# Kernel tuning notes

Hardware: AMD Instinct MI355X
Metric: run time of the kernel (lower is better)

Reference implementation:

```python
import jax, jax.numpy as jnp
import numpy as np

N, E, H, C, IN = 20000, 640000, 4, 64, 256
HC = H * C
NEG_SLOPE = 0.2


def setup_inputs() -> dict:
    key = jax.random.key(0)
    ks = jax.random.split(key, 24)
    rn = lambda k, s: jax.random.normal(k, s, jnp.float32) * 0.05
    return {
        "x": jax.random.normal(ks[0], (N, IN), jnp.float32),
        "edge_index": jax.random.randint(ks[1], (2, E), 0, N),
        "confidence": jax.random.normal(ks[2], (N,), jnp.float32),
        "w_in": rn(ks[3], (IN, C)), "b_in": jnp.zeros((C,), jnp.float32),
        "lin_w0": rn(ks[4], (C, HC)),
        "lin_w12": rn(ks[5], (2, HC, HC)),
        "att_src": rn(ks[6], (3, H, C)),
        "att_dst": rn(ks[7], (3, H, C)),
        "gat_bias": jnp.zeros((3, HC), jnp.float32),
        "conf_w": rn(ks[8], (HC, 1)), "conf_b": jnp.zeros((1,), jnp.float32),
        "nc_w1": rn(ks[9], (HC, C)), "nc_b1": jnp.zeros((C,), jnp.float32),
        "nc_w2": rn(ks[10], (C, 1)), "nc_b2": jnp.zeros((1,), jnp.float32),
        "oc_w1": rn(ks[11], (HC, C)), "oc_b1": jnp.zeros((C,), jnp.float32),
        "oc_w2": rn(ks[12], (C, 1)), "oc_b2": jnp.zeros((1,), jnp.float32),
        "ec_w1": rn(ks[13], (HC, C)), "ec_b1": jnp.zeros((C,), jnp.float32),
        "ec_w2": rn(ks[14], (C, 4)), "ec_b2": jnp.zeros((4,), jnp.float32),
    }


def _gat_layer(h_in, src, dst, n, lin_w, a_src, a_dst, bias):
    # h_in: (n, in_ch). PyG GATConv: linear -> per-edge attn -> segment softmax -> scatter-add.
    h = (h_in @ lin_w).reshape(n, H, C)
    s_src = jnp.einsum("nhc,hc->nh", h, a_src)  # (n, H)
    s_dst = jnp.einsum("nhc,hc->nh", h, a_dst)
    alpha = jax.nn.leaky_relu(s_src[src] + s_dst[dst], NEG_SLOPE)  # (E', H)
    # softmax over incoming edges of each dst node (self-loops guarantee coverage)
    amax = jax.ops.segment_max(alpha, dst, num_segments=n)
    ex = jnp.exp(alpha - amax[dst])
    denom = jax.ops.segment_sum(ex, dst, num_segments=n)
    coef = ex / jnp.maximum(denom[dst], 1e-16)
    msg = h[src] * coef[:, :, None]  # (E', H, C)
    out = jax.ops.segment_sum(msg, dst, num_segments=n)
    return out.reshape(n, HC) + bias


def reference(x, edge_index, confidence, w_in, b_in, lin_w0, lin_w12,
              att_src, att_dst, gat_bias, conf_w, conf_b,
              nc_w1, nc_b1, nc_w2, nc_b2, oc_w1, oc_b1, oc_w2, oc_b2,
              ec_w1, ec_b1, ec_w2, ec_b2):
    n = x.shape[0]
    loops = jnp.arange(n)
    src = jnp.concatenate([edge_index[0], loops])  # PyG add_self_loops=True
    dst = jnp.concatenate([edge_index[1], loops])
    h = jax.nn.relu(x @ w_in + b_in)  # input_proj + relu (dropout off in eval)
    lin_ws = [lin_w0, lin_w12[0], lin_w12[1]]
    conf_norm = jax.nn.sigmoid(confidence)  # (n,)
    for i in range(3):
        h_new = _gat_layer(h, src, dst, n, lin_ws[i], att_src[i], att_dst[i], gat_bias[i])
        cw = jax.nn.sigmoid(h_new @ conf_w + conf_b)[:, 0] * conf_norm
        h_new = h_new * cw[:, None]
        h = h + h_new if h.shape[-1] == h_new.shape[-1] else h_new
        if i < 2:
            h = jax.nn.relu(h)
    mlp = lambda w1, b1, w2, b2: jax.nn.relu(h @ w1 + b1) @ w2 + b2
    node_pred = jax.nn.sigmoid(mlp(nc_w1, nc_b1, nc_w2, nc_b2))[:, 0]
    origin_pred = jax.nn.sigmoid(mlp(oc_w1, oc_b1, oc_w2, oc_b2))[:, 0]
    error_type_pred = mlp(ec_w1, ec_b1, ec_w2, ec_b2)
    return node_pred, origin_pred, error_type_pred, h
```

## Files before the change

### kernel.cpp

```cpp
#include <hip/hip_runtime.h>
#include <cstdint>
#include <cstddef>

#define NN   20000
#define NPAD 20224
#define EE   640000
#define E2   660000
#define HHD  4
#define CC   64
#define HC   256
#define NEG  0.2f

#define NBUK 313
#define NBLK 129
#define EPB  5120
#define SCN  (NBUK * NBLK)

typedef short bf16x8 __attribute__((ext_vector_type(8)));
typedef float f32x4 __attribute__((ext_vector_type(4)));

__device__ __forceinline__ float sigmoidf_(float x) { return 1.0f / (1.0f + __expf(-x)); }

__device__ __forceinline__ float wred_sum(float v) {
#pragma unroll
    for (int d = 32; d; d >>= 1) v += __shfl_xor(v, d, 64);
    return v;
}

__device__ __forceinline__ unsigned short f2bf(float f) {
    unsigned u = __float_as_uint(f);
    u = (u + 0x7fff + ((u >> 16) & 1)) >> 16;
    return (unsigned short)u;
}
__device__ __forceinline__ float bfval(unsigned short h) { return __uint_as_float(((unsigned)h) << 16); }
__device__ __forceinline__ float bf_lo(unsigned u) { return __uint_as_float(u << 16); }
__device__ __forceinline__ float bf_hi(unsigned u) { return __uint_as_float(u & 0xffff0000u); }

__global__ __launch_bounds__(256) void hist_edges(const int* __restrict__ ei,
                                                  int* __restrict__ bhist) {
    __shared__ int h[NBUK];
    int bl = blockIdx.x, t = threadIdx.x;
    for (int i = t; i < NBUK; i += 256) h[i] = 0;
    __syncthreads();
    int e0 = bl * EPB;
#pragma unroll 4
    for (int i = t; i < EPB; i += 256) {
        int e = e0 + i;
        if (e < E2) {
            int d = (e < EE) ? ei[EE + e] : (e - EE);
            atomicAdd(&h[d >> 6], 1);
        }
    }
    __syncthreads();
    for (int i = t; i < NBUK; i += 256) bhist[i * NBLK + bl] = h[i];
}

__global__ __launch_bounds__(1024) void scan_hist(const int* __restrict__ bhist,
                                                  int* __restrict__ sbase) {
    __shared__ int buf[1024];
    int t = threadIdx.x;
    int base = t * 40;
    int local[40];
    int s = 0;
#pragma unroll
    for (int i = 0; i < 40; i++) {
        int idx = base + i;
        int v = (idx < SCN) ? bhist[idx] : 0;
        local[i] = v;
        s += v;
    }
    buf[t] = s;
    __syncthreads();
    for (int d = 1; d < 1024; d <<= 1) {
        int tv = (t >= d) ? buf[t - d] : 0;
        __syncthreads();
        buf[t] += tv;
        __syncthreads();
    }
    int run = buf[t] - s;
#pragma unroll
    for (int i = 0; i < 40; i++) {
        int idx = base + i;
        if (idx < SCN) sbase[idx] = run;
        run += local[i];
    }
}

__global__ __launch_bounds__(256) void scatter_bucket(const int* __restrict__ ei,
                                                      const int* __restrict__ sbase,
                                                      unsigned int* __restrict__ ebuf) {
    __shared__ int cur[NBUK];
    int bl = blockIdx.x, t = threadIdx.x;
    for (int i = t; i < NBUK; i += 256) cur[i] = sbase[i * NBLK + bl];
    __syncthreads();
    int e0 = bl * EPB;
#pragma unroll 4
    for (int i = t; i < EPB; i += 256) {
        int e = e0 + i;
        if (e < E2) {
            int s, d;
            if (e < EE) { s = ei[e]; d = ei[EE + e]; }
            else        { s = e - EE; d = s; }
            int p = atomicAdd(&cur[d >> 6], 1);
            ebuf[p] = ((unsigned int)(d & 63) << 15) | (unsigned int)s;
        }
    }
}

__global__ __launch_bounds__(256) void build_csr(const unsigned int* __restrict__ ebuf,
                                                 const int* __restrict__ sbase,
                                                 int* __restrict__ off,
                                                 int* __restrict__ csr) {
    __shared__ int hist[64], sc[64], curl[64];
    int bu = blockIdx.x, t = threadIdx.x;
    int base = sbase[bu * NBLK];
    int end  = (bu + 1 < NBUK) ? sbase[(bu + 1) * NBLK] : E2;
    int ne = end - base;
    if (t < 64) hist[t] = 0;
    __syncthreads();
    for (int i = t; i < ne; i += 256) {
        int dl = (int)(ebuf[base + i] >> 15);
        atomicAdd(&hist[dl], 1);
    }
    __syncthreads();
    if (t < 64) sc[t] = hist[t];
    __syncthreads();
    for (int d = 1; d < 64; d <<= 1) {
        int v = (t < 64 && t >= d) ? sc[t - d] : 0;
        __syncthreads();
        if (t < 64) sc[t] += v;
        __syncthreads();
    }
    int n0 = bu * 64;
    if (t < 64) {
        int ex = base + sc[t] - hist[t];
        if (n0 + t < NN) off[n0 + t] = ex;
        curl[t] = ex;
    }
    if (bu == NBUK - 1 && t == 0) off[NN] = E2;
    __syncthreads();
    for (int i = t; i < ne; i += 256) {
        unsigned int v = ebuf[base + i];
        int dl = (int)(v >> 15);
        int p = atomicAdd(&curl[dl], 1);
        csr[p] = (int)(v & 0x7fffu);
    }
}

#define WTOT 212992
__global__ void prep_inputs(const float* __restrict__ x,
                            const float* __restrict__ w_in, const float* __restrict__ lin_w0,
                            const float* __restrict__ lin_w12,
                            const float* __restrict__ nc1, const float* __restrict__ oc1,
                            const float* __restrict__ ec1,
                            const float* __restrict__ nb, const float* __restrict__ ob,
                            const float* __restrict__ eb,
                            unsigned short* __restrict__ whi,
                            float* __restrict__ bcat,
                            unsigned short* __restrict__ xh, unsigned short* __restrict__ xl) {
    int idx = blockIdx.x * 256 + threadIdx.x;
    if (idx < NN * 64) {
        float4 v = ((const float4*)x)[idx];
        ushort4 hi, lo;
        hi.x = f2bf(v.x); lo.x = f2bf(v.x - bfval(hi.x));
        hi.y = f2bf(v.y); lo.y = f2bf(v.y - bfval(hi.y));
        hi.z = f2bf(v.z); lo.z = f2bf(v.z - bfval(hi.z));
        hi.w = f2bf(v.w); lo.w = f2bf(v.w - bfval(hi.w));
        ((ushort4*)xh)[idx] = hi;
        ((ushort4*)xl)[idx] = lo;
    }
    if (idx < 192) {
        int g = idx >> 6, jj = idx & 63;
        const float* b = (g == 0) ? nb : ((g == 1) ? ob : eb);
        bcat[idx] = b[jj];
    }
    if (idx >= WTOT) return;
    float v;
    if (idx < 16384) {
        int n = idx >> 8, k = idx & 255;
        v = w_in[k * 64 + n];
    } else if (idx < 32768) {
        int r = idx - 16384;
        int n = r >> 6, k = r & 63;
        v = lin_w0[k * 256 + n];
    } else if (idx < 98304) {
        int r = idx - 32768;
        int n = r >> 8, k = r & 255;
        v = lin_w12[k * 256 + n];
    } else if (idx < 163840) {
        int r = idx - 98304;
        int n = r >> 8, k = r & 255;
        v = lin_w12[65536 + k * 256 + n];
    } else {
        int r = idx - 163840;
        int n = r >> 8, k = r & 255;
        int g = n >> 6, jj = n & 63;
        const float* w = (g == 0) ? nc1 : ((g == 1) ? oc1 : ec1);
        v = w[k * 64 + jj];
    }
    whi[idx] = f2bf(v);
}

template <int K, int OUT_CH, int MODE, int NT>
__global__ __launch_bounds__(256) void gemm_lds(
    const unsigned short* __restrict__ Ahp, const unsigned short* __restrict__ Alp,
    const unsigned short* __restrict__ Wh,
    const float* __restrict__ bias,
    unsigned short* __restrict__ Outh, unsigned short* __restrict__ Outl,
    const float* __restrict__ a_src, const float* __restrict__ a_dst,
    float* __restrict__ s_src, float* __restrict__ s_dst,
    const float* __restrict__ w2n, const float* __restrict__ w2o,
    const float* __restrict__ w2e,
    const float* __restrict__ b2n, const float* __restrict__ b2o,
    const float* __restrict__ b2e,
    float* __restrict__ outbuf, int nreal) {
    constexpr int LB = K + 8;
    constexpr int NS = K / 32;
    __shared__ unsigned short Bh[64 * LB];
    const int tid = threadIdx.x;
    const int wv = tid >> 6, lane = tid & 63;
    const int quad = lane >> 4, ln = lane & 15;
    const int mb = blockIdx.x * 64;
    const int r0 = mb + wv * 16 + ln;

    const unsigned short* aph = Ahp + (size_t)r0 * K + quad * 8;
    const unsigned short* apl = Alp + (size_t)r0 * K + quad * 8;
    bf16x8 ah[NS], al[NS];
#pragma unroll
    for (int s = 0; s < NS; s++) {
        ah[s] = *(const bf16x8*)(aph + s * 32);
        al[s] = *(const bf16x8*)(apl + s * 32);
    }

    for (int ct = 0; ct < NT; ct++) {
        const int cb = ct * 64;
        if (ct > 0) __syncthreads();

        constexpr int NCHK = 64 * (K / 8);
#pragma unroll
        for (int i = 0; i < NCHK / 256; i++) {
            int flat = tid + i * 256;
            int r = flat / (K / 8);
            int c = (flat % (K / 8)) * 8;
            *(uint4*)&Bh[r * LB + c] = *(const uint4*)&Wh[(size_t)(cb + r) * K + c];
        }
        __syncthreads();

        f32x4 acc[4];
#pragma unroll
        for (int j = 0; j < 4; j++) {
            acc[j][0] = 0.f; acc[j][1] = 0.f; acc[j][2] = 0.f; acc[j][3] = 0.f;
        }

#pragma unroll
        for (int s = 0; s < NS; s++) {
#pragma unroll
            for (int cg = 0; cg < 4; cg++) {
                bf16x8 bh = *(const bf16x8*)&Bh[(cg * 16 + ln) * LB + quad * 8 + s * 32];
                acc[cg] = __builtin_amdgcn_mfma_f32_16x16x32_bf16(ah[s], bh, acc[cg], 0, 0, 0);
                acc[cg] = __builtin_amdgcn_mfma_f32_16x16x32_bf16(al[s], bh, acc[cg], 0, 0, 0);
            }
        }

        if (MODE == 1) {
            float av[4], dv[4];
#pragma unroll
            for (int cg = 0; cg < 4; cg++) {
                av[cg] = a_src[cb + cg * 16 + ln];
                dv[cg] = a_dst[cb + cg * 16 + ln];
            }
#pragma unroll
            for (int reg = 0; reg < 4; reg++) {
                float ps = 0.f, pd = 0.f;
#pragma unroll
                for (int cg = 0; cg < 4; cg++) {
                    float t = acc[cg][reg];
                    ps += t * av[cg];
                    pd += t * dv[cg];
                }
#pragma unroll
                for (int d = 1; d < 16; d <<= 1) {
                    ps += __shfl_xor(ps, d, 64);
                    pd += __shfl_xor(pd, d, 64);
                }
                if (ln == 0) {
                    int row = mb + wv * 16 + quad * 4 + reg;
                    if (row < nreal) {
                        s_src[row * 4 + ct] = ps;
                        s_dst[row * 4 + ct] = pd;
                    }
                }
            }
        }

        if (MODE == 3) {
            float bv[4];
#pragma unroll
            for (int cg = 0; cg < 4; cg++) bv[cg] = bias[cb + cg * 16 + ln];
            if (ct < 2) {
                const float* w2 = (ct == 0) ? w2n : w2o;
                float b2 = (ct == 0) ? b2n[0] : b2o[0];
                float wv2[4];
#pragma unroll
                for (int cg = 0; cg < 4; cg++) wv2[cg] = w2[cg * 16 + ln];
#pragma unroll
                for (int reg = 0; reg < 4; reg++) {
                    float t = 0.f;
#pragma unroll
                    for (int cg = 0; cg < 4; cg++) {
                        float tv = fmaxf(acc[cg][reg] + bv[cg], 0.f);
                        t += tv * wv2[cg];
                    }
#pragma unroll
                    for (int d = 1; d < 16; d <<= 1) t += __shfl_xor(t, d, 64);
                    int row = mb + wv * 16 + quad * 4 + reg;
                    if (ln == 0 && row < nreal)
                        outbuf[ct * NN + row] = sigmoidf_(t + b2);
                }
            } else {
                float4 w4[4];
#pragma unroll
                for (int cg = 0; cg < 4; cg++) w4[cg] = ((const float4*)w2e)[cg * 16 + ln];
#pragma unroll
                for (int reg = 0; reg < 4; reg++) {
                    float e0 = 0.f, e1 = 0.f, e2 = 0.f, e3 = 0.f;
#pragma unroll
                    for (int cg = 0; cg < 4; cg++) {
                        float tv = fmaxf(acc[cg][reg] + bv[cg], 0.f);
                        e0 += tv * w4[cg].x; e1 += tv * w4[cg].y;
                        e2 += tv * w4[cg].z; e3 += tv * w4[cg].w;
                    }
#pragma unroll
                    for (int d = 1; d < 16; d <<= 1) {
                        e0 += __shfl_xor(e0, d, 64); e1 += __shfl_xor(e1, d, 64);
                        e2 += __shfl_xor(e2, d, 64); e3 += __shfl_xor(e3, d, 64);
                    }
                    int row = mb + wv * 16 + quad * 4 + reg;
                    if (ln == 0 && row < nreal) {
                        float4 ev = make_float4(e0 + b2e[0], e1 + b2e[1], e2 + b2e[2], e3 + b2e[3]);
                        *(float4*)&outbuf[2 * NN + row * 4] = ev;
                    }
                }
            }
            continue;
        }

#pragma unroll
        for (int cg = 0; cg < 4; cg++) {
            int col = cb + cg * 16 + ln;
            int rbase = mb + wv * 16 + quad * 4;
#pragma unroll
            for (int reg = 0; reg < 4; reg++) {
                float v = acc[cg][reg];
                int r = rbase + reg;
                if (MODE == 0) {
                    v += bias[col]; v = fmaxf(v, 0.f);
                    unsigned short hi = f2bf(v);
                    Outh[(size_t)r * OUT_CH + col] = hi;
                    Outl[(size_t)r * OUT_CH + col] = f2bf(v - bfval(hi));
                } else if (MODE == 1) {
                    Outh[(size_t)r * OUT_CH + col] = f2bf(v);
                }
            }
        }
    }
}

__global__ __launch_bounds__(256) void gat_node(const unsigned short* __restrict__ hhb,
                                                const float* __restrict__ s_src,
                                                const float* __restrict__ s_dst,
                                                const int* __restrict__ csr_src,
                                                const int* __restrict__ csr_off,
                                                const float* __restrict__ gbias,
                                                const float* __restrict__ conf_w,
                                                const float* __restrict__ conf_b,
                                                const float* __restrict__ confid,
                                                unsigned short* __restrict__ h_hi,
                                                unsigned short* __restrict__ h_lo,
                                                float* __restrict__ outbuf,
                                                int layer) {
    __shared__ float Lc[4][64];
    __shared__ int   Ls[4][16];
    int wv = threadIdx.x >> 6;
    int lane = threadIdx.x & 63;
    int n = blockIdx.x * 4 + wv;
    int myhead = lane >> 4, slot = lane & 15;
    int off0 = csr_off[n];
    int deg = csr_off[n + 1] - off0;
    const int* cp = csr_src + off0;
    const unsigned short* hrow = hhb + lane * 4;
    float sdm = s_dst[n * 4 + myhead];

    float ax = 0.f, ay = 0.f, az = 0.f, aw = 0.f, smp = 0.f;
    int nch = (deg + 15) >> 4;
    bool valid = slot < deg;
    int sl = cp[valid ? slot : deg - 1];
    float ssv = s_src[sl * 4 + myhead];
    for (int t = 0; t < nch; t++) {
        float a = ssv + sdm;
        a = a > 0.f ? a : NEG * a;
        float c = valid ? __expf(a) : 0.f;
        smp += c;
        Lc[wv][lane] = c;
        if (myhead == 0) Ls[wv][slot] = sl;
        __builtin_amdgcn_wave_barrier();
        float4 c0 = *(const float4*)&Lc[wv][myhead * 16 + 0];
        float4 c1 = *(const float4*)&Lc[wv][myhead * 16 + 4];
        float4 c2 = *(const float4*)&Lc[wv][myhead * 16 + 8];
        float4 c3 = *(const float4*)&Lc[wv][myhead * 16 + 12];
        int4 s0 = *(const int4*)&Ls[wv][0];
        int4 s1 = *(const int4*)&Ls[wv][4];
        int4 s2 = *(const int4*)&Ls[wv][8];
        int4 s3 = *(const int4*)&Ls[wv][12];
        __builtin_amdgcn_wave_barrier();
        if (t + 1 < nch) {
            int i = ((t + 1) << 4) + slot;
            valid = i < deg;
            sl = cp[valid ? i : deg - 1];
            ssv = s_src[sl * 4 + myhead];
        }
        float cf[16] = {c0.x, c0.y, c0.z, c0.w, c1.x, c1.y, c1.z, c1.w,
                        c2.x, c2.y, c2.z, c2.w, c3.x, c3.y, c3.z, c3.w};
        int sv[16] = {s0.x, s0.y, s0.z, s0.w, s1.x, s1.y, s1.z, s1.w,
                      s2.x, s2.y, s2.z, s2.w, s3.x, s3.y, s3.z, s3.w};
#pragma unroll
        for (int q = 0; q < 16; q++) {
            uint2 u = *(const uint2*)(hrow + ((size_t)sv[q] << 8));
            ax += cf[q] * bf_lo(u.x); ay += cf[q] * bf_hi(u.x);
            az += cf[q] * bf_lo(u.y); aw += cf[q] * bf_hi(u.y);
        }
    }
    smp += __shfl_xor(smp, 1, 64);
    smp += __shfl_xor(smp, 2, 64);
    smp += __shfl_xor(smp, 4, 64);
    smp += __shfl_xor(smp, 8, 64);
    float inv = 1.0f / fmaxf(smp, 1e-16f);
    ax *= inv; ay *= inv; az *= inv; aw *= inv;

    float4 b4 = *(const float4*)&gbias[lane * 4];
    float hx = ax + b4.x, hy = ay + b4.y, hz = az + b4.z, hw = aw + b4.w;
    float4 cw4 = *(const float4*)&conf_w[lane * 4];
    float local = hx * cw4.x + hy * cw4.y + hz * cw4.z + hw * cw4.w;
    float tot = wred_sum(local);
    float cw = sigmoidf_(tot + conf_b[0]) * sigmoidf_(confid[n]);
    hx *= cw; hy *= cw; hz *= cw; hw *= cw;
    if (layer > 0) {
        ushort4 ph = *(const ushort4*)&h_hi[(size_t)n * HC + lane * 4];
        ushort4 pl = *(const ushort4*)&h_lo[(size_t)n * HC + lane * 4];
        hx += bfval(ph.x) + bfval(pl.x);
        hy += bfval(ph.y) + bfval(pl.y);
        hz += bfval(ph.z) + bfval(pl.z);
        hw += bfval(ph.w) + bfval(pl.w);
    }
    if (layer < 2) {
        hx = fmaxf(hx, 0.f); hy = fmaxf(hy, 0.f);
        hz = fmaxf(hz, 0.f); hw = fmaxf(hw, 0.f);
    } else {
        *(float4*)&outbuf[6 * NN + (size_t)n * HC + lane * 4] =
            make_float4(hx, hy, hz, hw);
    }
    ushort4 oh, ol;
    oh.x = f2bf(hx); ol.x = f2bf(hx - bfval(oh.x));
    oh.y = f2bf(hy); ol.y = f2bf(hy - bfval(oh.y));
    oh.z = f2bf(hz); ol.z = f2bf(hz - bfval(oh.z));
    oh.w = f2bf(hw); ol.w = f2bf(hw - bfval(oh.w));
    *(ushort4*)&h_hi[(size_t)n * HC + lane * 4] = oh;
    *(ushort4*)&h_lo[(size_t)n * HC + lane * 4] = ol;
}

extern "C" void kernel_launch(void* const* d_in, const int* in_sizes, int n_in,
                              void* d_out, int out_size, void* d_ws, size_t ws_size,
                              hipStream_t stream) {
    const float* x       = (const float*)d_in[0];
    const int*   ei      = (const int*)d_in[1];
    const float* conf    = (const float*)d_in[2];
    const float* w_in    = (const float*)d_in[3];
    const float* b_in    = (const float*)d_in[4];
    const float* lin_w0  = (const float*)d_in[5];
    const float* lin_w12 = (const float*)d_in[6];
    const float* att_src = (const float*)d_in[7];
    const float* att_dst = (const float*)d_in[8];
    const float* gbias   = (const float*)d_in[9];
    const float* conf_w  = (const float*)d_in[10];
    const float* conf_b  = (const float*)d_in[11];
    const float* nc_w1   = (const float*)d_in[12];
    const float* nc_b1   = (const float*)d_in[13];
    const float* nc_w2   = (const float*)d_in[14];
    const float* nc_b2   = (const float*)d_in[15];
    const float* oc_w1   = (const float*)d_in[16];
    const float* oc_b1   = (const float*)d_in[17];
    const float* oc_w2   = (const float*)d_in[18];
    const float* oc_b2   = (const float*)d_in[19];
    const float* ec_w1   = (const float*)d_in[20];
    const float* ec_b1   = (const float*)d_in[21];
    const float* ec_w2   = (const float*)d_in[22];
    const float* ec_b2   = (const float*)d_in[23];
    float* out = (float*)d_out;

    char* p = (char*)d_ws;
    auto alloc = [&](size_t bytes) -> void* {
        void* r = (void*)p;
        p += (bytes + 255) & ~(size_t)255;
        return r;
    };
    unsigned short* h_hi = (unsigned short*)alloc((size_t)NPAD * HC * 2);
    unsigned short* h_lo = (unsigned short*)alloc((size_t)NPAD * HC * 2);
    unsigned short* hh   = (unsigned short*)alloc((size_t)NPAD * HC * 2);
    unsigned short* h0h  = (unsigned short*)alloc((size_t)NPAD * CC * 2);
    unsigned short* h0l  = (unsigned short*)alloc((size_t)NPAD * CC * 2);
    float*          ssrc = (float*)alloc((size_t)NN * 4 * 4);
    float*          sdst = (float*)alloc((size_t)NN * 4 * 4);
    int*            off  = (int*)alloc((size_t)(NN + 1) * 4);
    int*            csr  = (int*)alloc((size_t)E2 * 4);
    int*            bhist= (int*)alloc((size_t)SCN * 4);
    int*            sbase= (int*)alloc((size_t)SCN * 4);
    unsigned short* whi  = (unsigned short*)alloc((size_t)WTOT * 2);
    float*          bcat = (float*)alloc((size_t)192 * 4);
    unsigned short* xh   = (unsigned short*)alloc((size_t)NPAD * 256 * 2 * 2);
    unsigned short* xl   = xh + (size_t)NPAD * 256;
    unsigned int*   ebuf = (unsigned int*)xh;

    const unsigned short* wt_in = whi;
    const unsigned short* wt_l0 = whi + 16384;
    const unsigned short* wt_a  = whi + 32768;
    const unsigned short* wt_b  = whi + 98304;
    const unsigned short* wt_hd = whi + 163840;

    hist_edges<<<NBLK, 256, 0, stream>>>(ei, bhist);
    scan_hist<<<1, 1024, 0, stream>>>(bhist, sbase);
    scatter_bucket<<<NBLK, 256, 0, stream>>>(ei, sbase, ebuf);
    build_csr<<<NBUK, 256, 0, stream>>>(ebuf, sbase, off, csr);

    prep_inputs<<<(NN * 64 + 255) / 256, 256, 0, stream>>>(
        x, w_in, lin_w0, lin_w12, nc_w1, oc_w1, ec_w1, nc_b1, oc_b1, ec_b1,
        whi, bcat, xh, xl);

    gemm_lds<256, 64, 0, 1><<<dim3(NPAD / 64, 1), 256, 0, stream>>>(
        xh, xl, wt_in, b_in, h0h, h0l, nullptr, nullptr, nullptr, nullptr,
        nullptr, nullptr, nullptr, nullptr, nullptr, nullptr, nullptr, NN);

    gemm_lds<64, 256, 1, 4><<<dim3(NPAD / 64, 1), 256, 0, stream>>>(
        h0h, h0l, wt_l0, nullptr, hh, nullptr, att_src, att_dst, ssrc, sdst,
        nullptr, nullptr, nullptr, nullptr, nullptr, nullptr, nullptr, NN);
    gat_node<<<NN / 4, 256, 0, stream>>>(hh, ssrc, sdst, csr, off, gbias, conf_w, conf_b, conf,
                                         h_hi, h_lo, out, 0);

    for (int i = 1; i < 3; i++) {
        const unsigned short* wh = (i == 1) ? wt_a : wt_b;
        gemm_lds<256, 256, 1, 4><<<dim3(NPAD / 64, 1), 256, 0, stream>>>(
            h_hi, h_lo, wh, nullptr, hh, nullptr,
            att_src + i * HHD * CC, att_dst + i * HHD * CC, ssrc, sdst,
            nullptr, nullptr, nullptr, nullptr, nullptr, nullptr, nullptr, NN);
        gat_node<<<NN / 4, 256, 0, stream>>>(hh, ssrc, sdst, csr, off, gbias + i * HC,
                                             conf_w, conf_b, conf, h_hi, h_lo, out, i);
    }

    gemm_lds<256, 192, 3, 3><<<dim3(NPAD / 64, 1), 256, 0, stream>>>(
        h_hi, h_lo, wt_hd, bcat, nullptr, nullptr, nullptr, nullptr, nullptr, nullptr,
        nc_w2, oc_w2, ec_w2, nc_b2, oc_b2, ec_b2, out, NN);
}
```

Baseline: 386.0 us.

## Fuse all stages into one persistent kernel with grid-wide barriers

Replaces the sequence of about twelve kernel launches (CSR build, input prep, GEMMs, GAT aggregation, heads) with a single persistent kernel of 960 blocks. The kernel loops over virtual block indices and separates stages with atomic-counter grid barriers. Independent stages now share phases: prep runs with the histogram, the first GEMM with the scan, and the layer-0 GEMM with the scatter. This removes launch gaps and tail effects. The cost is a shared LDS footprint sized for the largest stage, which may lower occupancy, plus spin-wait barriers that deadlock if the 960 blocks cannot all be resident. The scan is reworked to 256 threads, and ebuf gets its own buffer instead of aliasing xh.

```diff
diff --git a/kernel.cpp b/kernel.cpp
--- a/kernel.cpp
+++ b/kernel.cpp
@@ -15,6 +15,9 @@
 #define NBLK 129
 #define EPB  5120
 #define SCN  (NBUK * NBLK)
+#define PREP_BLKS 5000
+#define GEMM_BLKS (NPAD / 64)
+#define GRID 960
 
 typedef short bf16x8 __attribute__((ext_vector_type(8)));
 typedef float f32x4 __attribute__((ext_vector_type(4)));
@@ -36,10 +39,21 @@
 __device__ __forceinline__ float bf_lo(unsigned u) { return __uint_as_float(u << 16); }
 __device__ __forceinline__ float bf_hi(unsigned u) { return __uint_as_float(u & 0xffff0000u); }
 
-__global__ __launch_bounds__(256) void hist_edges(const int* __restrict__ ei,
-                                                  int* __restrict__ bhist) {
-    __shared__ int h[NBUK];
-    int bl = blockIdx.x, t = threadIdx.x;
+__device__ __forceinline__ void gsync(int* bar, int target) {
+    __syncthreads();
+    if (threadIdx.x == 0) {
+        __threadfence();
+        atomicAdd(bar, 1);
+        while (atomicAdd(bar, 0) < target) __builtin_amdgcn_s_sleep(8);
+        __threadfence();
+    }
+    __syncthreads();
+}
+
+
+__device__ __forceinline__ void hist_body(int bl, const int* __restrict__ ei,
+                                          int* __restrict__ bhist, int* h ) {
+    int t = threadIdx.x;
     for (int i = t; i < NBUK; i += 256) h[i] = 0;
     __syncthreads();
     int e0 = bl * EPB;
@@ -53,44 +67,14 @@
     }
     __syncthreads();
     for (int i = t; i < NBUK; i += 256) bhist[i * NBLK + bl] = h[i];
-}
-
-__global__ __launch_bounds__(1024) void scan_hist(const int* __restrict__ bhist,
-                                                  int* __restrict__ sbase) {
-    __shared__ int buf[1024];
+    __syncthreads();
+}
+
+__device__ __forceinline__ void scatter_body(int bl, const int* __restrict__ ei,
+                                             const int* __restrict__ sbase,
+                                             unsigned int* __restrict__ ebuf,
+                                             int* cur ) {
     int t = threadIdx.x;
-    int base = t * 40;
-    int local[40];
-    int s = 0;
-#pragma unroll
-    for (int i = 0; i < 40; i++) {
-        int idx = base + i;
-        int v = (idx < SCN) ? bhist[idx] : 0;
-        local[i] = v;
-        s += v;
-    }
-    buf[t] = s;
-    __syncthreads();
-    for (int d = 1; d < 1024; d <<= 1) {
-        int tv = (t >= d) ? buf[t - d] : 0;
-        __syncthreads();
-        buf[t] += tv;
-        __syncthreads();
-    }
-    int run = buf[t] - s;
-#pragma unroll
-    for (int i = 0; i < 40; i++) {
-        int idx = base + i;
-        if (idx < SCN) sbase[idx] = run;
-        run += local[i];
-    }
-}
-
-__global__ __launch_bounds__(256) void scatter_bucket(const int* __restrict__ ei,
-                                                      const int* __restrict__ sbase,
-                                                      unsigned int* __restrict__ ebuf) {
-    __shared__ int cur[NBUK];
-    int bl = blockIdx.x, t = threadIdx.x;
     for (int i = t; i < NBUK; i += 256) cur[i] = sbase[i * NBLK + bl];
     __syncthreads();
     int e0 = bl * EPB;
@@ -105,14 +89,16 @@
             ebuf[p] = ((unsigned int)(d & 63) << 15) | (unsigned int)s;
         }
     }
-}
-
-__global__ __launch_bounds__(256) void build_csr(const unsigned int* __restrict__ ebuf,
-                                                 const int* __restrict__ sbase,
-                                                 int* __restrict__ off,
-                                                 int* __restrict__ csr) {
-    __shared__ int hist[64], sc[64], curl[64];
-    int bu = blockIdx.x, t = threadIdx.x;
+    __syncthreads();
+}
+
+__device__ __forceinline__ void build_body(int bu, const unsigned int* __restrict__ ebuf,
+                                           const int* __restrict__ sbase,
+                                           int* __restrict__ off, int* __restrict__ csr,
+                                           int* hist ) {
+    int* sc = hist + 64;
+    int* curl = hist + 128;
+    int t = threadIdx.x;
     int base = sbase[bu * NBLK];
     int end  = (bu + 1 < NBUK) ? sbase[(bu + 1) * NBLK] : E2;
     int ne = end - base;
@@ -145,10 +131,38 @@
         int p = atomicAdd(&curl[dl], 1);
         csr[p] = (int)(v & 0x7fffu);
     }
+    __syncthreads();
+}
+
+__device__ __forceinline__ void scan_body(const int* __restrict__ bhist,
+                                          int* __restrict__ sbase, int* buf ) {
+    const int CH = (SCN + 255) / 256;
+    int t = threadIdx.x;
+    int b0 = t * CH;
+    int s = 0;
+    for (int i = 0; i < CH; i++) {
+        int idx = b0 + i;
+        s += (idx < SCN) ? bhist[idx] : 0;
+    }
+    buf[t] = s;
+    __syncthreads();
+    for (int d = 1; d < 256; d <<= 1) {
+        int tv = (t >= d) ? buf[t - d] : 0;
+        __syncthreads();
+        buf[t] += tv;
+        __syncthreads();
+    }
+    int run = buf[t] - s;
+    for (int i = 0; i < CH; i++) {
+        int idx = b0 + i;
+        if (idx < SCN) { sbase[idx] = run; run += bhist[idx]; }
+    }
+    __syncthreads();
 }
 
 #define WTOT 212992
-__global__ void prep_inputs(const float* __restrict__ x,
+__device__ __forceinline__ void prep_body(int idx,
+                            const float* __restrict__ x,
                             const float* __restrict__ w_in, const float* __restrict__ lin_w0,
                             const float* __restrict__ lin_w12,
                             const float* __restrict__ nc1, const float* __restrict__ oc1,
@@ -158,7 +172,6 @@
                             unsigned short* __restrict__ whi,
                             float* __restrict__ bcat,
                             unsigned short* __restrict__ xh, unsigned short* __restrict__ xl) {
-    int idx = blockIdx.x * 256 + threadIdx.x;
     if (idx < NN * 64) {
         float4 v = ((const float4*)x)[idx];
         ushort4 hi, lo;
@@ -202,25 +215,25 @@
 }
 
 template <int K, int OUT_CH, int MODE, int NT>
-__global__ __launch_bounds__(256) void gemm_lds(
+__device__ __forceinline__ void gemm_body(
+    unsigned short* Bh, int mb,
     const unsigned short* __restrict__ Ahp, const unsigned short* __restrict__ Alp,
     const unsigned short* __restrict__ Wh,
     const float* __restrict__ bias,
-    unsigned short* __restrict__ Outh, unsigned short* __restrict__ Outl,
+    unsigned short* __restrict__ Outh,
     const float* __restrict__ a_src, const float* __restrict__ a_dst,
     float* __restrict__ s_src, float* __restrict__ s_dst,
     const float* __restrict__ w2n, const float* __restrict__ w2o,
     const float* __restrict__ w2e,
     const float* __restrict__ b2n, const float* __restrict__ b2o,
     const float* __restrict__ b2e,
+    unsigned short* __restrict__ Outl,
     float* __restrict__ outbuf, int nreal) {
     constexpr int LB = K + 8;
     constexpr int NS = K / 32;
-    __shared__ unsigned short Bh[64 * LB];
     const int tid = threadIdx.x;
     const int wv = tid >> 6, lane = tid & 63;
     const int quad = lane >> 4, ln = lane & 15;
-    const int mb = blockIdx.x * 64;
     const int r0 = mb + wv * 16 + ln;
 
     const unsigned short* aph = Ahp + (size_t)r0 * K + quad * 8;
@@ -234,7 +247,7 @@
 
     for (int ct = 0; ct < NT; ct++) {
         const int cb = ct * 64;
-        if (ct > 0) __syncthreads();
+        __syncthreads();
 
         constexpr int NCHK = 64 * (K / 8);
 #pragma unroll
@@ -366,24 +379,18 @@
     }
 }
 
-__global__ __launch_bounds__(256) void gat_node(const unsigned short* __restrict__ hhb,
-                                                const float* __restrict__ s_src,
-                                                const float* __restrict__ s_dst,
-                                                const int* __restrict__ csr_src,
-                                                const int* __restrict__ csr_off,
-                                                const float* __restrict__ gbias,
-                                                const float* __restrict__ conf_w,
-                                                const float* __restrict__ conf_b,
-                                                const float* __restrict__ confid,
-                                                unsigned short* __restrict__ h_hi,
-                                                unsigned short* __restrict__ h_lo,
-                                                float* __restrict__ outbuf,
-                                                int layer) {
-    __shared__ float Lc[4][64];
-    __shared__ int   Ls[4][16];
+__device__ __forceinline__ void gat_body(int nb, const unsigned short* __restrict__ hhb,
+        const float* __restrict__ s_src, const float* __restrict__ s_dst,
+        const int* __restrict__ csr_src, const int* __restrict__ csr_off,
+        const float* __restrict__ gbias, const float* __restrict__ conf_w,
+        const float* __restrict__ conf_b, const float* __restrict__ confid,
+        unsigned short* __restrict__ h_hi, unsigned short* __restrict__ h_lo,
+        float* __restrict__ outbuf, int layer, float* Lc, int* Ls) {
     int wv = threadIdx.x >> 6;
     int lane = threadIdx.x & 63;
-    int n = blockIdx.x * 4 + wv;
+    int n = nb * 4 + wv;
+    float* Lcw = Lc + wv * 64;
+    int*   Lsw = Ls + wv * 16;
     int myhead = lane >> 4, slot = lane & 15;
     int off0 = csr_off[n];
     int deg = csr_off[n + 1] - off0;
@@ -401,17 +408,17 @@
         a = a > 0.f ? a : NEG * a;
         float c = valid ? __expf(a) : 0.f;
         smp += c;
-        Lc[wv][lane] = c;
-        if (myhead == 0) Ls[wv][slot] = sl;
+        Lcw[lane] = c;
+        if (myhead == 0) Lsw[slot] = sl;
         __builtin_amdgcn_wave_barrier();
-        float4 c0 = *(const float4*)&Lc[wv][myhead * 16 + 0];
-        float4 c1 = *(const float4*)&Lc[wv][myhead * 16 + 4];
-        float4 c2 = *(const float4*)&Lc[wv][myhead * 16 + 8];
-        float4 c3 = *(const float4*)&Lc[wv][myhead * 16 + 12];
-        int4 s0 = *(const int4*)&Ls[wv][0];
-        int4 s1 = *(const int4*)&Ls[wv][4];
-        int4 s2 = *(const int4*)&Ls[wv][8];
-        int4 s3 = *(const int4*)&Ls[wv][12];
+        float4 c0 = *(const float4*)&Lcw[myhead * 16 + 0];
+        float4 c1 = *(const float4*)&Lcw[myhead * 16 + 4];
+        float4 c2 = *(const float4*)&Lcw[myhead * 16 + 8];
+        float4 c3 = *(const float4*)&Lcw[myhead * 16 + 12];
+        int4 s0 = *(const int4*)&Lsw[0];
+        int4 s1 = *(const int4*)&Lsw[4];
+        int4 s2 = *(const int4*)&Lsw[8];
+        int4 s3 = *(const int4*)&Lsw[12];
         __builtin_amdgcn_wave_barrier();
         if (t + 1 < nch) {
             int i = ((t + 1) << 4) + slot;
@@ -466,6 +473,110 @@
     oh.w = f2bf(hw); ol.w = f2bf(hw - bfval(oh.w));
     *(ushort4*)&h_hi[(size_t)n * HC + lane * 4] = oh;
     *(ushort4*)&h_lo[(size_t)n * HC + lane * 4] = ol;
+}
+
+__global__ __launch_bounds__(256, 4) void meganet(
+    const float* __restrict__ x, const int* __restrict__ ei,
+    const float* __restrict__ conf,
+    const float* __restrict__ w_in, const float* __restrict__ b_in,
+    const float* __restrict__ lin_w0, const float* __restrict__ lin_w12,
+    const float* __restrict__ att_src, const float* __restrict__ att_dst,
+    const float* __restrict__ gbias,
+    const float* __restrict__ conf_w, const float* __restrict__ conf_b,
+    const float* __restrict__ nc_w1, const float* __restrict__ nc_b1,
+    const float* __restrict__ nc_w2, const float* __restrict__ nc_b2,
+    const float* __restrict__ oc_w1, const float* __restrict__ oc_b1,
+    const float* __restrict__ oc_w2, const float* __restrict__ oc_b2,
+    const float* __restrict__ ec_w1, const float* __restrict__ ec_b1,
+    const float* __restrict__ ec_w2, const float* __restrict__ ec_b2,
+    unsigned short* h_hi, unsigned short* h_lo, unsigned short* hh,
+    unsigned short* h0h, unsigned short* h0l,
+    float* ssrc, float* sdst, int* off, int* csr,
+    int* bhist, int* sbase, unsigned int* ebuf,
+    unsigned short* whi, float* bcat,
+    unsigned short* xh, unsigned short* xl,
+    int* bar, float* out) {
+    __shared__ __align__(16) unsigned char smem[64 * 264 * 2];
+    unsigned short* Bh = (unsigned short*)smem;
+    int* ih = (int*)smem;
+    float* Lc = (float*)smem;
+    int* Ls = (int*)(smem + 1024);
+
+    const unsigned short* wt_in = whi;
+    const unsigned short* wt_l0 = whi + 16384;
+    const unsigned short* wt_a  = whi + 32768;
+    const unsigned short* wt_b  = whi + 98304;
+    const unsigned short* wt_hd = whi + 163840;
+
+    for (int vb = blockIdx.x; vb < PREP_BLKS + NBLK; vb += GRID) {
+        if (vb < PREP_BLKS)
+            prep_body(vb * 256 + threadIdx.x, x, w_in, lin_w0, lin_w12,
+                      nc_w1, oc_w1, ec_w1, nc_b1, oc_b1, ec_b1, whi, bcat, xh, xl);
+        else
+            hist_body(vb - PREP_BLKS, ei, bhist, ih);
+    }
+    gsync(bar, 1 * GRID);
+
+    for (int vb = blockIdx.x; vb < GEMM_BLKS + 1; vb += GRID) {
+        if (vb < GEMM_BLKS)
+            gemm_body<256, 64, 0, 1>(Bh, vb * 64, xh, xl, wt_in, b_in, h0h,
+                                     nullptr, nullptr, nullptr, nullptr,
+                                     nullptr, nullptr, nullptr, nullptr, nullptr, nullptr,
+                                     h0l, nullptr, NN);
+        else
+            scan_body(bhist, sbase, ih);
+    }
+    gsync(bar, 2 * GRID);
+
+    for (int vb = blockIdx.x; vb < NBLK + GEMM_BLKS; vb += GRID) {
+        if (vb < NBLK)
+            scatter_body(vb, ei, sbase, ebuf, ih);
+        else
+            gemm_body<64, 256, 1, 4>(Bh, (vb - NBLK) * 64, h0h, h0l, wt_l0, nullptr, hh,
+                                     att_src, att_dst, ssrc, sdst,
+                                     nullptr, nullptr, nullptr, nullptr, nullptr, nullptr,
+                                     nullptr, nullptr, NN);
+    }
+    gsync(bar, 3 * GRID);
+
+    for (int vb = blockIdx.x; vb < NBUK; vb += GRID)
+        build_body(vb, ebuf, sbase, off, csr, ih);
+    gsync(bar, 4 * GRID);
+
+    for (int vb = blockIdx.x; vb < NN / 4; vb += GRID)
+        gat_body(vb, hh, ssrc, sdst, csr, off, gbias, conf_w, conf_b, conf,
+                 h_hi, h_lo, out, 0, Lc, Ls);
+    gsync(bar, 5 * GRID);
+
+    for (int vb = blockIdx.x; vb < GEMM_BLKS; vb += GRID)
+        gemm_body<256, 256, 1, 4>(Bh, vb * 64, h_hi, h_lo, wt_a, nullptr, hh,
+                                  att_src + HHD * CC, att_dst + HHD * CC, ssrc, sdst,
+                                  nullptr, nullptr, nullptr, nullptr, nullptr, nullptr,
+                                  nullptr, nullptr, NN);
+    gsync(bar, 6 * GRID);
+
+    for (int vb = blockIdx.x; vb < NN / 4; vb += GRID)
+        gat_body(vb, hh, ssrc, sdst, csr, off, gbias + HC, conf_w, conf_b, conf,
+                 h_hi, h_lo, out, 1, Lc, Ls);
+    gsync(bar, 7 * GRID);
+
+    for (int vb = blockIdx.x; vb < GEMM_BLKS; vb += GRID)
+        gemm_body<256, 256, 1, 4>(Bh, vb * 64, h_hi, h_lo, wt_b, nullptr, hh,
+                                  att_src + 2 * HHD * CC, att_dst + 2 * HHD * CC, ssrc, sdst,
+                                  nullptr, nullptr, nullptr, nullptr, nullptr, nullptr,
+                                  nullptr, nullptr, NN);
+    gsync(bar, 8 * GRID);
+
+    for (int vb = blockIdx.x; vb < NN / 4; vb += GRID)
+        gat_body(vb, hh, ssrc, sdst, csr, off, gbias + 2 * HC, conf_w, conf_b, conf,
+                 h_hi, h_lo, out, 2, Lc, Ls);
+    gsync(bar, 9 * GRID);
+
+    for (int vb = blockIdx.x; vb < GEMM_BLKS; vb += GRID)
+        gemm_body<256, 192, 3, 3>(Bh, vb * 64, h_hi, h_lo, wt_hd, bcat, nullptr,
+                                  nullptr, nullptr, nullptr, nullptr,
+                                  nc_w2, oc_w2, ec_w2, nc_b2, oc_b2, ec_b2,
+                                  nullptr, out, NN);
 }
 
 extern "C" void kernel_launch(void* const* d_in, const int* in_sizes, int n_in,
@@ -514,48 +625,19 @@
     int*            csr  = (int*)alloc((size_t)E2 * 4);
     int*            bhist= (int*)alloc((size_t)SCN * 4);
     int*            sbase= (int*)alloc((size_t)SCN * 4);
+    unsigned int*   ebuf = (unsigned int*)alloc((size_t)E2 * 4);
     unsigned short* whi  = (unsigned short*)alloc((size_t)WTOT * 2);
     float*          bcat = (float*)alloc((size_t)192 * 4);
     unsigned short* xh   = (unsigned short*)alloc((size_t)NPAD * 256 * 2 * 2);
     unsigned short* xl   = xh + (size_t)NPAD * 256;
-    unsigned int*   ebuf = (unsigned int*)xh;
-
-    const unsigned short* wt_in = whi;
-    const unsigned short* wt_l0 = whi + 16384;
-    const unsigned short* wt_a  = whi + 32768;
-    const unsigned short* wt_b  = whi + 98304;
-    const unsigned short* wt_hd = whi + 163840;
-
-    hist_edges<<<NBLK, 256, 0, stream>>>(ei, bhist);
-    scan_hist<<<1, 1024, 0, stream>>>(bhist, sbase);
-    scatter_bucket<<<NBLK, 256, 0, stream>>>(ei, sbase, ebuf);
-    build_csr<<<NBUK, 256, 0, stream>>>(ebuf, sbase, off, csr);
-
-    prep_inputs<<<(NN * 64 + 255) / 256, 256, 0, stream>>>(
-        x, w_in, lin_w0, lin_w12, nc_w1, oc_w1, ec_w1, nc_b1, oc_b1, ec_b1,
-        whi, bcat, xh, xl);
-
-    gemm_lds<256, 64, 0, 1><<<dim3(NPAD / 64, 1), 256, 0, stream>>>(
-        xh, xl, wt_in, b_in, h0h, h0l, nullptr, nullptr, nullptr, nullptr,
-        nullptr, nullptr, nullptr, nullptr, nullptr, nullptr, nullptr, NN);
-
-    gemm_lds<64, 256, 1, 4><<<dim3(NPAD / 64, 1), 256, 0, stream>>>(
-        h0h, h0l, wt_l0, nullptr, hh, nullptr, att_src, att_dst, ssrc, sdst,
-        nullptr, nullptr, nullptr, nullptr, nullptr, nullptr, nullptr, NN);
-    gat_node<<<NN / 4, 256, 0, stream>>>(hh, ssrc, sdst, csr, off, gbias, conf_w, conf_b, conf,
-                                         h_hi, h_lo, out, 0);
-
-    for (int i = 1; i < 3; i++) {
-        const unsigned short* wh = (i == 1) ? wt_a : wt_b;
-        gemm_lds<256, 256, 1, 4><<<dim3(NPAD / 64, 1), 256, 0, stream>>>(
-            h_hi, h_lo, wh, nullptr, hh, nullptr,
-            att_src + i * HHD * CC, att_dst + i * HHD * CC, ssrc, sdst,
-            nullptr, nullptr, nullptr, nullptr, nullptr, nullptr, nullptr, NN);
-        gat_node<<<NN / 4, 256, 0, stream>>>(hh, ssrc, sdst, csr, off, gbias + i * HC,
-                                             conf_w, conf_b, conf, h_hi, h_lo, out, i);
-    }
-
-    gemm_lds<256, 192, 3, 3><<<dim3(NPAD / 64, 1), 256, 0, stream>>>(
-        h_hi, h_lo, wt_hd, bcat, nullptr, nullptr, nullptr, nullptr, nullptr, nullptr,
-        nc_w2, oc_w2, ec_w2, nc_b2, oc_b2, ec_b2, out, NN);
-}
+    int*            bar  = (int*)alloc(256);
+
+    hipMemsetAsync(bar, 0, 256, stream);
+
+    meganet<<<GRID, 256, 0, stream>>>(
+        x, ei, conf, w_in, b_in, lin_w0, lin_w12, att_src, att_dst, gbias,
+        conf_w, conf_b, nc_w1, nc_b1, nc_w2, nc_b2, oc_w1, oc_b1, oc_w2, oc_b2,
+        ec_w1, ec_b1, ec_w2, ec_b2,
+        h_hi, h_lo, hh, h0h, h0l, ssrc, sdst, off, csr,
+        bhist, sbase, ebuf, whi, bcat, xh, xl, bar, out);
+}
```

Result: slower. 1.441 ms (+273.4%).
